# Performance work log

Hardware: AMD Instinct MI355X
Metric: run time of the kernel (lower is better)

Reference implementation:

```python
import jax, jax.numpy as jnp
import numpy as np
from jax import lax

B, S, D, H, TMAX = 8, 512, 256, 4, 20
DH = D // H
LAMBDA = 1e-3
V_TH = 1.0


def setup_inputs() -> dict:
    key = jax.random.key(0)
    ks = jax.random.split(key, 10)
    sc = lambda n: 1.0 / np.sqrt(n)
    f32 = jnp.float32
    return {
        "x": jax.random.normal(ks[0], (B, S, D), f32),
        "Wq": (jax.random.normal(ks[1], (D, D), f32) * sc(D)),
        "Wk": (jax.random.normal(ks[2], (D, D), f32) * sc(D)),
        "Wv": (jax.random.normal(ks[3], (D, D), f32) * sc(D)),
        "Wo": (jax.random.normal(ks[4], (D, D), f32) * sc(D)),
        "bo": jnp.zeros((D,), f32),
        "Wg1": (jax.random.normal(ks[5], (D, 32), f32) * sc(D)),
        "bg1": jnp.zeros((32,), f32),
        "Wg2": (jax.random.normal(ks[6], (32, 1), f32) * sc(32)),
        "bg2": jnp.zeros((1,), f32),
        "alpha_q": jnp.asarray(np.exp(-1 / 5.0), f32),
        "beta_q": jnp.asarray(np.exp(-1 / 20.0), f32),
        "alpha_k": jnp.asarray(np.exp(-1 / 5.0), f32),
        "beta_k": jnp.asarray(np.exp(-1 / 20.0), f32),
        "alpha_v": jnp.asarray(np.exp(-1 / 5.0), f32),
        "beta_v": jnp.asarray(np.exp(-1 / 20.0), f32),
    }


def _lif_spikes(x, alpha, beta, Ti):
    """LIF recurrence with CONSTANT input x per step, sequential only over T.
    x: [B,S,D], Ti: [B,S] int. Returns spikes [B,S,TMAX,D], zeroed for t >= Ti
    (equivalent to the original per-(b,s) loop that only runs Ti steps,
    since the recurrence is causal)."""
    zeros = jnp.zeros_like(x)
    tmask = jnp.arange(TMAX)

    def step(carry, t):
        v, i = carry
        i = alpha * i + x
        v = beta * v + i
        spk = (v >= V_TH).astype(x.dtype)
        v = v * (1.0 - spk)  # v_reset = 0
        spk_out = spk * (t < Ti).astype(x.dtype)[..., None]
        return (v, i), spk_out

    _, spks = lax.scan(step, (zeros, zeros), tmask)
    return jnp.moveaxis(spks, 0, 2)  # [B,S,T,D]


def reference(x, Wq, Wk, Wv, Wo, bo, Wg1, bg1, Wg2, bg2,
              alpha_q, beta_q, alpha_k, beta_k, alpha_v, beta_v):
    q = x @ Wq
    k = x @ Wk
    v = x @ Wv
    # adaptive window gate -> Ti in [1, TMAX]
    gate = jax.nn.sigmoid(jax.nn.relu(x @ Wg1 + bg1) @ Wg2 + bg2)[..., 0]  # [B,S]
    Ti = jnp.clip(jnp.ceil(gate * TMAX), 1, TMAX).astype(jnp.int32)
    q_spk = _lif_spikes(q, alpha_q, beta_q, Ti)  # [B,S,T,D]
    k_spk = _lif_spikes(k, alpha_k, beta_k, Ti)
    v_spk = _lif_spikes(v, alpha_v, beta_v, Ti)
    qh = q_spk.reshape(B, S, TMAX, H, DH)
    kh = k_spk.reshape(B, S, TMAX, H, DH)
    vh = v_spk.reshape(B, S, TMAX, H, DH)
    scale = DH ** -0.5
    Sraw = jnp.einsum('bithd,bjthd->bhij', qh, kh) * scale  # [B,H,S,S]
    W = jax.nn.softmax(Sraw, axis=-1)
    v_mean = vh.mean(axis=2)  # [B,S,H,DH] (mean over full T, zeros beyond Ti)
    out = jnp.einsum('bhij,bjhd->bihd', W, v_mean).reshape(B, S, D)
    out = out @ Wo + bo
    reg = LAMBDA * Ti.astype(jnp.float32).mean()
    return out, reg, Ti, W
```

## Files before the change

kernel.cpp:

```cpp
#include <hip/hip_runtime.h>
#include <hip/hip_bf16.h>

typedef unsigned long long u64;
typedef unsigned short u16;
typedef __attribute__((ext_vector_type(8))) short short8;
typedef __attribute__((ext_vector_type(4))) float float4_t;

#define BB 8
#define SS 512
#define DD 256
#define HH 4
#define TT 20
#define BS (BB*SS)

#define REG_OFF (BS*DD)
#define TI_OFF  (REG_OFF+1)
#define W_OFF   (TI_OFF+BS)

static __device__ __forceinline__ u16 f2bf(float f) {
    __hip_bfloat16 h = __float2bfloat16(f);
    return *reinterpret_cast<u16*>(&h);
}

__global__ __launch_bounds__(256) void k_gate(
    const float* __restrict__ x,
    const float* __restrict__ Wg1, const float* __restrict__ bg1,
    const float* __restrict__ Wg2, const float* __restrict__ bg2,
    float* __restrict__ ti_out)
{
    __shared__ float wgl[DD*32];
    __shared__ float xl[16][DD];
    const int tid  = threadIdx.x;
    const int tok0 = blockIdx.x * 16;

    #pragma unroll
    for (int i = 0; i < 8; ++i) {
        int j = i*256 + tid;
        *reinterpret_cast<float4_t*>(&wgl[j*4]) =
            *reinterpret_cast<const float4_t*>(&Wg1[j*4]);
    }
    #pragma unroll
    for (int m = 0; m < 16; ++m) xl[m][tid] = x[(size_t)(tok0+m)*DD + tid];
    __syncthreads();

    const int tok = tid >> 4;
    const int cq  = tid & 15;
    const int c   = cq * 2;
    float a0 = 0.f, a1 = 0.f;
    #pragma unroll 8
    for (int r = 0; r < DD; ++r) {
        float xv = xl[tok][r];
        a0 += xv * wgl[r*32 + c];
        a1 += xv * wgl[r*32 + c + 1];
    }
    a0 += bg1[c]; a1 += bg1[c+1];
    a0 = a0 > 0.f ? a0 : 0.f;
    a1 = a1 > 0.f ? a1 : 0.f;
    float term = a0 * Wg2[c] + a1 * Wg2[c+1];
    #pragma unroll
    for (int msk = 8; msk >= 1; msk >>= 1) term += __shfl_xor(term, msk, 64);
    if (cq == 0) {
        float g  = term + bg2[0];
        float sg = 1.f / (1.f + expf(-g));
        int ti = (int)ceilf(sg * (float)TT);
        ti = ti < 1 ? 1 : (ti > TT ? TT : ti);
        ti_out[tok0 + tok] = (float)ti;
    }
}

__global__ __launch_bounds__(256) void k_proj_lif(
    const float* __restrict__ x, const float* __restrict__ Wq,
    const float* __restrict__ Wk, const float* __restrict__ Wv,
    const float* __restrict__ aq, const float* __restrict__ bq_,
    const float* __restrict__ ak, const float* __restrict__ bk_,
    const float* __restrict__ av, const float* __restrict__ bv_,
    const float* __restrict__ ti_in,
    u64* __restrict__ qpack, u64* __restrict__ kpack,
    u16* __restrict__ vmbT)
{
    __shared__ __align__(16) union {
        float xt[DD][16];
        float ax[16][DD];
    } sm;
    __shared__ int til[16];
    const int tid  = threadIdx.x;
    const int proj = blockIdx.y;
    const int tok0 = blockIdx.x * 16;

    #pragma unroll
    for (int m = 0; m < 16; ++m) sm.xt[tid][m] = x[(size_t)(tok0+m)*DD + tid];
    if (tid < 16) til[tid] = (int)ti_in[tok0 + tid];
    __syncthreads();

    const float* W    = proj == 0 ? Wq  : (proj == 1 ? Wk  : Wv);
    const float alpha = proj == 0 ? *aq : (proj == 1 ? *ak : *av);
    const float beta  = proj == 0 ? *bq_: (proj == 1 ? *bk_: *bv_);

    const int c  = tid & 63;
    const int tg = tid >> 6;

    float4_t acc[4];
    #pragma unroll
    for (int i = 0; i < 4; ++i) acc[i] = (float4_t){0.f, 0.f, 0.f, 0.f};

    const float* Wp = W + c*4;
    #pragma unroll 8
    for (int r = 0; r < DD; ++r) {
        float4_t wf = *reinterpret_cast<const float4_t*>(Wp + (size_t)r*DD);
        float4_t xv = *reinterpret_cast<const float4_t*>(&sm.xt[r][tg*4]);
        acc[0] += wf*xv.x; acc[1] += wf*xv.y; acc[2] += wf*xv.z; acc[3] += wf*xv.w;
    }
    __syncthreads();
    #pragma unroll
    for (int i = 0; i < 4; ++i)
        *reinterpret_cast<float4_t*>(&sm.ax[tg*4 + i][c*4]) = acc[i];
    __syncthreads();

    float val[16];
    #pragma unroll
    for (int m = 0; m < 16; ++m) val[m] = sm.ax[m][tid];

    const int lane = tid & 63;
    const int h    = tid >> 6;
    if (proj < 2) {
        u64* pack = (proj == 0) ? qpack : kpack;
        for (int m = 0; m < 16; ++m) {
            const int ti = til[m];
            float vv = 0.f, cur = 0.f;
            u64 myw = 0ull;
            #pragma unroll
            for (int t = 0; t < TT; ++t) {
                cur = alpha*cur + val[m];
                vv  = beta*vv + cur;
                bool s = (vv >= 1.f);
                u64 bal = __ballot(s);
                if (s) vv = 0.f;
                if (lane == t && t < ti) myw = bal;
            }
            if (lane < TT)
                pack[((size_t)(tok0+m)*HH + h)*TT + lane] = myw;
        }
    } else {
        u16 tmp[16];
        for (int m = 0; m < 16; ++m) {
            const int ti = til[m];
            float vv = 0.f, cur = 0.f, cnt = 0.f;
            #pragma unroll
            for (int t = 0; t < TT; ++t) {
                cur = alpha*cur + val[m];
                vv  = beta*vv + cur;
                bool s = (vv >= 1.f);
                if (s) { vv = 0.f; if (t < ti) cnt += 1.f; }
            }
            tmp[m] = f2bf(cnt * 0.05f);
        }
        *reinterpret_cast<short8*>(&vmbT[(size_t)tid*BS + tok0    ]) =
            *reinterpret_cast<short8*>(&tmp[0]);
        *reinterpret_cast<short8*>(&vmbT[(size_t)tid*BS + tok0 + 8]) =
            *reinterpret_cast<short8*>(&tmp[8]);
    }
}

__global__ __launch_bounds__(256) void k_attn(
    const u64* __restrict__ qpack, const u64* __restrict__ kpack,
    const u16* __restrict__ vmbT,
    float* __restrict__ Wout, float* __restrict__ attn)
{
    __shared__ u64 ql[16][TT];
    __shared__ __align__(16) u16 CP[16*SS];
    const int tid  = threadIdx.x;
    const int tile = blockIdx.x & 31;
    const int h    = (blockIdx.x >> 5) & 3;
    const int b    = blockIdx.x >> 7;
    const int i0   = tile * 16;
    const int lane = tid & 63, wv = tid >> 6;

    for (int idx = tid; idx < 16*TT; idx += 256) {
        int i = idx / TT, t = idx - i*TT;
        ql[i][t] = qpack[((size_t)(b*SS + i0 + i)*HH + h)*TT + t];
    }

    u64 kr0[TT], kr1[TT];
    {
        const u64* kp0 = &kpack[((size_t)(b*SS + tid      )*HH + h)*TT];
        const u64* kp1 = &kpack[((size_t)(b*SS + tid + 256)*HH + h)*TT];
        #pragma unroll
        for (int t = 0; t < TT; ++t) { kr0[t] = kp0[t]; kr1[t] = kp1[t]; }
    }
    __syncthreads();

    for (int i = 0; i < 16; ++i) {
        int c0 = 0, c1 = 0;
        #pragma unroll
        for (int t = 0; t < TT; ++t) {
            u64 q = ql[i][t];
            c0 += __popcll(q & kr0[t]);
            c1 += __popcll(q & kr1[t]);
        }
        CP[i*SS + tid]       = (u16)c0;
        CP[i*SS + tid + 256] = (u16)c1;
    }
    __syncthreads();

    for (int rr = 0; rr < 4; ++rr) {
        const int i = wv*4 + rr;
        float sv[8];
        float m = -1e30f;
        #pragma unroll
        for (int k2 = 0; k2 < 8; ++k2) {
            sv[k2] = (float)CP[i*SS + lane + 64*k2] * 0.125f;
            m = fmaxf(m, sv[k2]);
        }
        #pragma unroll
        for (int msk = 32; msk >= 1; msk >>= 1) m = fmaxf(m, __shfl_xor(m, msk, 64));
        float sum = 0.f;
        #pragma unroll
        for (int k2 = 0; k2 < 8; ++k2) { sv[k2] = expf(sv[k2] - m); sum += sv[k2]; }
        #pragma unroll
        for (int msk = 32; msk >= 1; msk >>= 1) sum += __shfl_xor(sum, msk, 64);
        float inv = 1.f / sum;
        size_t wbase = ((size_t)((b*HH + h)*SS) + i0 + i) * SS;
        #pragma unroll
        for (int k2 = 0; k2 < 8; ++k2) {
            int j = lane + 64*k2;
            float wval = sv[k2] * inv;
            Wout[wbase + j] = wval;
            CP[(i*SS + j) ^ ((i & 7) << 3)] = f2bf(wval);
        }
    }
    __syncthreads();

    const int n0 = wv * 16;
    const int mr = lane & 15;
    const int g  = lane >> 4;
    float4_t acc = {0.f, 0.f, 0.f, 0.f};
    const u16* vbT = vmbT + (size_t)(h*64 + n0 + mr)*BS + b*SS;
    for (int ks = 0; ks < 16; ++ks) {
        int k = ks*32 + g*8;
        int aidx = (mr*SS + k) ^ ((mr & 7) << 3);
        short8 afrag = *reinterpret_cast<const short8*>(&CP[aidx]);
        short8 bfrag = *reinterpret_cast<const short8*>(vbT + k);
        acc = __builtin_amdgcn_mfma_f32_16x16x32_bf16(afrag, bfrag, acc, 0, 0, 0);
    }
    #pragma unroll
    for (int r = 0; r < 4; ++r) {
        int row = g*4 + r;
        attn[(size_t)(b*SS + i0 + row)*DD + h*64 + n0 + mr] = acc[r];
    }
}

__global__ __launch_bounds__(256) void k_outproj(
    const float* __restrict__ attn, const float* __restrict__ Wo,
    const float* __restrict__ bo, const float* __restrict__ ti,
    float* __restrict__ out)
{
    __shared__ __align__(16) union {
        float xt[DD][16];
        float ax[16][DD];
    } sm;
    __shared__ float ps[4];
    const int tid  = threadIdx.x;
    const int tok0 = blockIdx.x * 16;

    #pragma unroll
    for (int m = 0; m < 16; ++m) sm.xt[tid][m] = attn[(size_t)(tok0+m)*DD + tid];
    __syncthreads();

    const int c  = tid & 63;
    const int tg = tid >> 6;

    float4_t acc[4];
    #pragma unroll
    for (int i = 0; i < 4; ++i) acc[i] = (float4_t){0.f, 0.f, 0.f, 0.f};
    const float* Wp = Wo + c*4;
    #pragma unroll 8
    for (int r = 0; r < DD; ++r) {
        float4_t wf = *reinterpret_cast<const float4_t*>(Wp + (size_t)r*DD);
        float4_t xv = *reinterpret_cast<const float4_t*>(&sm.xt[r][tg*4]);
        acc[0] += wf*xv.x; acc[1] += wf*xv.y; acc[2] += wf*xv.z; acc[3] += wf*xv.w;
    }
    __syncthreads();
    #pragma unroll
    for (int i = 0; i < 4; ++i)
        *reinterpret_cast<float4_t*>(&sm.ax[tg*4 + i][c*4]) = acc[i];
    __syncthreads();

    float bb = bo[tid];
    #pragma unroll
    for (int m = 0; m < 16; ++m)
        out[(size_t)(tok0+m)*DD + tid] = sm.ax[m][tid] + bb;

    if (blockIdx.x == 0) {
        float s = 0.f;
        for (int m = 0; m < 16; ++m) s += ti[m*256 + tid];
        #pragma unroll
        for (int msk = 32; msk >= 1; msk >>= 1) s += __shfl_xor(s, msk, 64);
        if ((tid & 63) == 0) ps[tid >> 6] = s;
        __syncthreads();
        if (tid == 0) out[REG_OFF] = 1e-3f * (ps[0]+ps[1]+ps[2]+ps[3]) / 4096.f;
    }
}

extern "C" void kernel_launch(void* const* d_in, const int* in_sizes, int n_in,
                              void* d_out, int out_size, void* d_ws, size_t ws_size,
                              hipStream_t stream)
{
    (void)in_sizes; (void)n_in; (void)out_size; (void)ws_size;
    const float* x   = (const float*)d_in[0];
    const float* Wq  = (const float*)d_in[1];
    const float* Wk  = (const float*)d_in[2];
    const float* Wv  = (const float*)d_in[3];
    const float* Wo  = (const float*)d_in[4];
    const float* bo  = (const float*)d_in[5];
    const float* Wg1 = (const float*)d_in[6];
    const float* bg1 = (const float*)d_in[7];
    const float* Wg2 = (const float*)d_in[8];
    const float* bg2 = (const float*)d_in[9];
    const float* aq  = (const float*)d_in[10];
    const float* bq  = (const float*)d_in[11];
    const float* ak  = (const float*)d_in[12];
    const float* bk  = (const float*)d_in[13];
    const float* av  = (const float*)d_in[14];
    const float* bv  = (const float*)d_in[15];
    float* out = (float*)d_out;

    u64* qp = (u64*)d_ws;
    u64* kp = qp + (size_t)BS*HH*TT;
    u16* vmbT = (u16*)(kp + (size_t)BS*HH*TT);
    float* attnbuf = (float*)(vmbT + (size_t)BS*DD);

    k_gate<<<256, 256, 0, stream>>>(x, Wg1, bg1, Wg2, bg2, out + TI_OFF);
    dim3 gproj(256, 3);
    k_proj_lif<<<gproj, 256, 0, stream>>>(x, Wq, Wk, Wv,
        aq, bq, ak, bk, av, bv, out + TI_OFF, qp, kp, vmbT);
    k_attn<<<1024, 256, 0, stream>>>(qp, kp, vmbT, out + W_OFF, attnbuf);
    k_outproj<<<256, 256, 0, stream>>>(attnbuf, Wo, bo, out + TI_OFF, out);
}
```

Measured before the change: 114.2 us.

## Halve tokens per block in projections and rewrite gate as wave-per-token

The projection+LIF and output-projection kernels now process 8 tokens per block instead of 16, doubling the grid to fill more compute units. The gate kernel is restructured so each wavefront handles one token, reading Wg1 directly from global memory rather than staging it in shared memory. This aims to improve occupancy and remove a large per-block LDS staging cost. The trade-off is halved weight reuse per block, which increases weight traffic through the caches.

Result: slower. 124.5 us (+9.1%).

```diff
diff --git a/kernel.cpp b/kernel.cpp
--- a/kernel.cpp
+++ b/kernel.cpp
@@ -4,6 +4,7 @@
 typedef unsigned long long u64;
 typedef unsigned short u16;
 typedef __attribute__((ext_vector_type(8))) short short8;
+typedef __attribute__((ext_vector_type(2))) float float2_t;
 typedef __attribute__((ext_vector_type(4))) float float4_t;
 
 #define BB 8
@@ -28,43 +29,33 @@
     const float* __restrict__ Wg2, const float* __restrict__ bg2,
     float* __restrict__ ti_out)
 {
-    __shared__ float wgl[DD*32];
-    __shared__ float xl[16][DD];
     const int tid  = threadIdx.x;
-    const int tok0 = blockIdx.x * 16;
-
-    #pragma unroll
-    for (int i = 0; i < 8; ++i) {
-        int j = i*256 + tid;
-        *reinterpret_cast<float4_t*>(&wgl[j*4]) =
-            *reinterpret_cast<const float4_t*>(&Wg1[j*4]);
-    }
-    #pragma unroll
-    for (int m = 0; m < 16; ++m) xl[m][tid] = x[(size_t)(tok0+m)*DD + tid];
-    __syncthreads();
-
-    const int tok = tid >> 4;
-    const int cq  = tid & 15;
-    const int c   = cq * 2;
-    float a0 = 0.f, a1 = 0.f;
-    #pragma unroll 8
-    for (int r = 0; r < DD; ++r) {
-        float xv = xl[tok][r];
-        a0 += xv * wgl[r*32 + c];
-        a1 += xv * wgl[r*32 + c + 1];
-    }
-    a0 += bg1[c]; a1 += bg1[c+1];
-    a0 = a0 > 0.f ? a0 : 0.f;
-    a1 = a1 > 0.f ? a1 : 0.f;
-    float term = a0 * Wg2[c] + a1 * Wg2[c+1];
-    #pragma unroll
-    for (int msk = 8; msk >= 1; msk >>= 1) term += __shfl_xor(term, msk, 64);
-    if (cq == 0) {
+    const int tok  = blockIdx.x * 4 + (tid >> 6);
+    const int lane = tid & 63;
+    const int c    = lane & 31;
+    const int half = lane >> 5;
+
+    const float* xr = x + (size_t)tok*DD + half*128;
+    const float* wg = Wg1 + (size_t)half*128*32 + c;
+    float acc = 0.f;
+    #pragma unroll 4
+    for (int i = 0; i < 32; ++i) {
+        float4_t xv = *reinterpret_cast<const float4_t*>(xr + i*4);
+        acc += xv.x * wg[(i*4+0)*32] + xv.y * wg[(i*4+1)*32]
+             + xv.z * wg[(i*4+2)*32] + xv.w * wg[(i*4+3)*32];
+    }
+    acc += __shfl_xor(acc, 32, 64);
+    acc += bg1[c];
+    float hrelu = acc > 0.f ? acc : 0.f;
+    float term  = hrelu * Wg2[c];
+    #pragma unroll
+    for (int msk = 16; msk >= 1; msk >>= 1) term += __shfl_xor(term, msk, 64);
+    if (lane == 0) {
         float g  = term + bg2[0];
         float sg = 1.f / (1.f + expf(-g));
         int ti = (int)ceilf(sg * (float)TT);
         ti = ti < 1 ? 1 : (ti > TT ? TT : ti);
-        ti_out[tok0 + tok] = (float)ti;
+        ti_out[tok] = (float)ti;
     }
 }
 
@@ -79,17 +70,17 @@
     u16* __restrict__ vmbT)
 {
     __shared__ __align__(16) union {
-        float xt[DD][16];
-        float ax[16][DD];
+        float xt[DD][8];
+        float ax[8][DD];
     } sm;
-    __shared__ int til[16];
+    __shared__ int til[8];
     const int tid  = threadIdx.x;
     const int proj = blockIdx.y;
-    const int tok0 = blockIdx.x * 16;
-
-    #pragma unroll
-    for (int m = 0; m < 16; ++m) sm.xt[tid][m] = x[(size_t)(tok0+m)*DD + tid];
-    if (tid < 16) til[tid] = (int)ti_in[tok0 + tid];
+    const int tok0 = blockIdx.x * 8;
+
+    #pragma unroll
+    for (int m = 0; m < 8; ++m) sm.xt[tid][m] = x[(size_t)(tok0+m)*DD + tid];
+    if (tid < 8) til[tid] = (int)ti_in[tok0 + tid];
     __syncthreads();
 
     const float* W    = proj == 0 ? Wq  : (proj == 1 ? Wk  : Wv);
@@ -99,32 +90,31 @@
     const int c  = tid & 63;
     const int tg = tid >> 6;
 
-    float4_t acc[4];
-    #pragma unroll
-    for (int i = 0; i < 4; ++i) acc[i] = (float4_t){0.f, 0.f, 0.f, 0.f};
+    float4_t acc[2];
+    acc[0] = (float4_t){0.f, 0.f, 0.f, 0.f};
+    acc[1] = (float4_t){0.f, 0.f, 0.f, 0.f};
 
     const float* Wp = W + c*4;
     #pragma unroll 8
     for (int r = 0; r < DD; ++r) {
         float4_t wf = *reinterpret_cast<const float4_t*>(Wp + (size_t)r*DD);
-        float4_t xv = *reinterpret_cast<const float4_t*>(&sm.xt[r][tg*4]);
-        acc[0] += wf*xv.x; acc[1] += wf*xv.y; acc[2] += wf*xv.z; acc[3] += wf*xv.w;
-    }
-    __syncthreads();
-    #pragma unroll
-    for (int i = 0; i < 4; ++i)
-        *reinterpret_cast<float4_t*>(&sm.ax[tg*4 + i][c*4]) = acc[i];
-    __syncthreads();
-
-    float val[16];
-    #pragma unroll
-    for (int m = 0; m < 16; ++m) val[m] = sm.ax[m][tid];
+        float2_t xv = *reinterpret_cast<const float2_t*>(&sm.xt[r][tg*2]);
+        acc[0] += wf*xv.x; acc[1] += wf*xv.y;
+    }
+    __syncthreads();
+    *reinterpret_cast<float4_t*>(&sm.ax[tg*2    ][c*4]) = acc[0];
+    *reinterpret_cast<float4_t*>(&sm.ax[tg*2 + 1][c*4]) = acc[1];
+    __syncthreads();
+
+    float val[8];
+    #pragma unroll
+    for (int m = 0; m < 8; ++m) val[m] = sm.ax[m][tid];
 
     const int lane = tid & 63;
     const int h    = tid >> 6;
     if (proj < 2) {
         u64* pack = (proj == 0) ? qpack : kpack;
-        for (int m = 0; m < 16; ++m) {
+        for (int m = 0; m < 8; ++m) {
             const int ti = til[m];
             float vv = 0.f, cur = 0.f;
             u64 myw = 0ull;
@@ -141,8 +131,8 @@
                 pack[((size_t)(tok0+m)*HH + h)*TT + lane] = myw;
         }
     } else {
-        u16 tmp[16];
-        for (int m = 0; m < 16; ++m) {
+        u16 tmp[8];
+        for (int m = 0; m < 8; ++m) {
             const int ti = til[m];
             float vv = 0.f, cur = 0.f, cnt = 0.f;
             #pragma unroll
@@ -154,10 +144,8 @@
             }
             tmp[m] = f2bf(cnt * 0.05f);
         }
-        *reinterpret_cast<short8*>(&vmbT[(size_t)tid*BS + tok0    ]) =
+        *reinterpret_cast<short8*>(&vmbT[(size_t)tid*BS + tok0]) =
             *reinterpret_cast<short8*>(&tmp[0]);
-        *reinterpret_cast<short8*>(&vmbT[(size_t)tid*BS + tok0 + 8]) =
-            *reinterpret_cast<short8*>(&tmp[8]);
     }
 }
 
@@ -255,39 +243,38 @@
     float* __restrict__ out)
 {
     __shared__ __align__(16) union {
-        float xt[DD][16];
-        float ax[16][DD];
+        float xt[DD][8];
+        float ax[8][DD];
     } sm;
     __shared__ float ps[4];
     const int tid  = threadIdx.x;
-    const int tok0 = blockIdx.x * 16;
-
-    #pragma unroll
-    for (int m = 0; m < 16; ++m) sm.xt[tid][m] = attn[(size_t)(tok0+m)*DD + tid];
+    const int tok0 = blockIdx.x * 8;
+
+    #pragma unroll
+    for (int m = 0; m < 8; ++m) sm.xt[tid][m] = attn[(size_t)(tok0+m)*DD + tid];
     __syncthreads();
 
     const int c  = tid & 63;
     const int tg = tid >> 6;
 
-    float4_t acc[4];
-    #pragma unroll
-    for (int i = 0; i < 4; ++i) acc[i] = (float4_t){0.f, 0.f, 0.f, 0.f};
+    float4_t acc[2];
+    acc[0] = (float4_t){0.f, 0.f, 0.f, 0.f};
+    acc[1] = (float4_t){0.f, 0.f, 0.f, 0.f};
     const float* Wp = Wo + c*4;
     #pragma unroll 8
     for (int r = 0; r < DD; ++r) {
         float4_t wf = *reinterpret_cast<const float4_t*>(Wp + (size_t)r*DD);
-        float4_t xv = *reinterpret_cast<const float4_t*>(&sm.xt[r][tg*4]);
-        acc[0] += wf*xv.x; acc[1] += wf*xv.y; acc[2] += wf*xv.z; acc[3] += wf*xv.w;
-    }
-    __syncthreads();
-    #pragma unroll
-    for (int i = 0; i < 4; ++i)
-        *reinterpret_cast<float4_t*>(&sm.ax[tg*4 + i][c*4]) = acc[i];
+        float2_t xv = *reinterpret_cast<const float2_t*>(&sm.xt[r][tg*2]);
+        acc[0] += wf*xv.x; acc[1] += wf*xv.y;
+    }
+    __syncthreads();
+    *reinterpret_cast<float4_t*>(&sm.ax[tg*2    ][c*4]) = acc[0];
+    *reinterpret_cast<float4_t*>(&sm.ax[tg*2 + 1][c*4]) = acc[1];
     __syncthreads();
 
     float bb = bo[tid];
     #pragma unroll
-    for (int m = 0; m < 16; ++m)
+    for (int m = 0; m < 8; ++m)
         out[(size_t)(tok0+m)*DD + tid] = sm.ax[m][tid] + bb;
 
     if (blockIdx.x == 0) {
@@ -329,10 +316,10 @@
     u16* vmbT = (u16*)(kp + (size_t)BS*HH*TT);
     float* attnbuf = (float*)(vmbT + (size_t)BS*DD);
 
-    k_gate<<<256, 256, 0, stream>>>(x, Wg1, bg1, Wg2, bg2, out + TI_OFF);
-    dim3 gproj(256, 3);
+    k_gate<<<1024, 256, 0, stream>>>(x, Wg1, bg1, Wg2, bg2, out + TI_OFF);
+    dim3 gproj(512, 3);
     k_proj_lif<<<gproj, 256, 0, stream>>>(x, Wq, Wk, Wv,
         aq, bq, ak, bk, av, bv, out + TI_OFF, qp, kp, vmbT);
     k_attn<<<1024, 256, 0, stream>>>(qp, kp, vmbT, out + W_OFF, attnbuf);
-    k_outproj<<<256, 256, 0, stream>>>(attnbuf, Wo, bo, out + TI_OFF, out);
-}
+    k_outproj<<<512, 256, 0, stream>>>(attnbuf, Wo, bo, out + TI_OFF, out);
+}
```
